# Kernel tuning notes

Hardware: AMD Instinct MI355X
Metric: run time of the kernel (lower is better)

## Reference

```python
import jax, jax.numpy as jnp
import numpy as np

B, S, H = 1, 4096, 2048
NH, HD = 16, 128  # num_heads, head_dim = H // NH


def setup_inputs() -> dict:
    key = jax.random.key(0)
    k1, k2, k3 = jax.random.split(key, 3)
    x = jax.random.normal(k1, (B, S, H), dtype=jnp.float32)
    w_qkv = jax.random.normal(k2, (3 * H, H), dtype=jnp.float32) * (1.0 / np.sqrt(H))
    w_out = jax.random.normal(k3, (H, H), dtype=jnp.float32) * (1.0 / np.sqrt(H))
    return {"x": x, "w_qkv": w_qkv, "w_out": w_out}


def reference(x, w_qkv, w_out):
    b, s, _ = x.shape
    # qkv projection: torch Linear computes x @ W^T
    qkv = jnp.einsum('bsh,oh->bso', x, w_qkv)
    qkv = qkv.reshape(b, s, 3, NH, HD).transpose(2, 0, 3, 1, 4)  # [3,B,NH,S,HD]
    q, k, v = qkv[0], qkv[1], qkv[2]
    # world_size == 1 -> single ring step == full attention with online softmax
    scores = jnp.einsum('bhqd,bhkd->bhqk', q, k) / np.sqrt(HD)
    m = jnp.max(scores, axis=-1, keepdims=True)          # running max (single step)
    p = jnp.exp(scores - m)                              # scores_exp
    out = jnp.einsum('bhqk,bhkd->bhqd', p, v)
    denom = jnp.sum(p, axis=-1, keepdims=True) + 1e-8    # running_sum + eps
    out = out / denom
    out = out.transpose(0, 2, 1, 3).reshape(b, s, H)     # [B,S,H]
    return jnp.einsum('bsh,oh->bso', out, w_out)
```

## Files before the change

### kernel.cpp

```cpp
#include <hip/hip_runtime.h>
#include <stdint.h>

typedef __attribute__((ext_vector_type(4))) float f32x4;
typedef __attribute__((ext_vector_type(16))) float f32x16;
typedef __attribute__((ext_vector_type(8))) short bf16x8;
typedef unsigned short u16;

#define MFMA(a, b, c) __builtin_amdgcn_mfma_f32_16x16x32_bf16(a, b, c, 0, 0, 0)
#define MFMA32(a, b, c) __builtin_amdgcn_mfma_f32_32x32x16_bf16(a, b, c, 0, 0, 0)
#define EXP2(x) __builtin_amdgcn_exp2f(x)
#define FENCE asm volatile("" ::: "memory")
#define BARRIER do { FENCE; __builtin_amdgcn_s_barrier(); FENCE; } while (0)

__device__ __forceinline__ u16 f2bf(float f) {
  union { float f; unsigned u; } x; x.f = f;
  unsigned r = x.u + 0x7fffu + ((x.u >> 16) & 1u);
  return (u16)(r >> 16);
}

__device__ __forceinline__ unsigned cvtpk(float lo, float hi) {
  unsigned r;
  asm("v_cvt_pk_bf16_f32 %0, %1, %2" : "=v"(r) : "v"(lo), "v"(hi));
  return r;
}

__device__ __forceinline__ void pl32swap(unsigned& a, unsigned& b) {
  asm volatile("v_permlane32_swap_b32 %0, %1" : "+v"(a), "+v"(b));
}

__device__ __forceinline__ void gload16(const void* g, void* l) {
  __builtin_amdgcn_global_load_lds(
      (const __attribute__((address_space(1))) unsigned int*)g,
      (__attribute__((address_space(3))) unsigned int*)l, 16, 0, 0);
}

__global__ void __launch_bounds__(256) cast_bf16(const float* __restrict__ in,
                                                 u16* __restrict__ out, int n4) {
  int i = blockIdx.x * 256 + threadIdx.x;
  if (i >= n4) return;
  float4 v = reinterpret_cast<const float4*>(in)[i];
  ushort4 o;
  o.x = f2bf(v.x); o.y = f2bf(v.y); o.z = f2bf(v.z); o.w = f2bf(v.w);
  reinterpret_cast<ushort4*>(out)[i] = o;
}

template <int EPI>
__global__ void __launch_bounds__(512)
gemm8(const u16* __restrict__ A, const u16* __restrict__ B,
      void* __restrict__ C0, void* __restrict__ C1, void* __restrict__ C2,
      int M, int N, int K, int MBt) {
  __shared__ alignas(16) char smb[98304];
  const int tid = threadIdx.x;
  const int w = tid >> 6, lane = tid & 63;
  const int lr = lane & 15, g = lane >> 4;
  const int wm = w >> 2, wn = w & 3;
  const int gb = (blockIdx.x & 7) * ((int)gridDim.x >> 3) + (blockIdx.x >> 3);
  const int mb = gb % MBt, nb = gb / MBt;
  const int m0 = mb * 128, n0 = nb * 256;
  const int NT = K >> 6, NIT = NT >> 1;

  const int l8 = lane >> 3, l7 = lane & 7;
  const int csb = (l7 ^ l8) * 16;
  const char* asrc;
  unsigned adst;
  {
    int r = (w & 3) * 8 + ((w >> 2) << 6) + l8;
    asrc = (const char*)(A + (size_t)(m0 + r) * K) + csb;
    adst = (unsigned)(r * 128 + l7 * 16);
  }
  const char* bsrcb[2];
  unsigned bdst[2];
#pragma unroll
  for (int j = 0; j < 2; ++j) {
    int c = 2 * w + j;
    int r = (c & 3) * 8 + ((c >> 2) << 6) + l8;
    bsrcb[j] = (const char*)(B + (size_t)(n0 + r) * K) + csb;
    bdst[j] = (unsigned)(r * 128 + l7 * 16);
  }
  const size_t row32 = (size_t)32 * K * 2;

#define STG(kt, u)                                                               \
  do {                                                                           \
    if ((kt) < NT) {                                                             \
      size_t _ko = (size_t)(kt) * 128;                                           \
      int _da = ((kt) & 1) ? 16384 : 0;                                          \
      int _db = 32768 + (((kt) & 1) ? 32768 : 0);                                \
      if ((u) == 0) {                                                            \
        gload16(asrc + _ko, smb + _da + adst);                                   \
      } else if ((u) == 1) {                                                     \
        gload16(bsrcb[0] + _ko, smb + _db + bdst[0]);                            \
        gload16(bsrcb[1] + _ko, smb + _db + bdst[1]);                            \
      } else if ((u) == 2) {                                                     \
        gload16(asrc + row32 + _ko, smb + _da + 4096 + adst);                    \
      } else {                                                                   \
        gload16(bsrcb[0] + row32 + _ko, smb + _db + 4096 + bdst[0]);             \
        gload16(bsrcb[1] + row32 + _ko, smb + _db + 4096 + bdst[1]);             \
      }                                                                          \
    }                                                                            \
  } while (0)

  f32x4 acc[4][4];
#pragma unroll
  for (int x = 0; x < 4; ++x)
#pragma unroll
    for (int y = 0; y < 4; ++y) acc[x][y] = f32x4{0.f, 0.f, 0.f, 0.f};
  bf16x8 af[2][2], bf01[2][2], bf23[2][2];
  const int aoff0 = ((g) ^ (lr & 7)) << 4;
  const int aoff1 = ((4 + g) ^ (lr & 7)) << 4;
  const int arowb = (wm * 64 + lr) * 128;
  const int browb = (wn * 64 + lr) * 128;

  auto LDA = [&](const char* base, int mih) {
#pragma unroll
    for (int mi = 0; mi < 2; ++mi) {
      const char* p = base + arowb + (mih * 32 + mi * 16) * 128;
      af[mi][0] = *(const bf16x8*)(p + aoff0);
      af[mi][1] = *(const bf16x8*)(p + aoff1);
    }
  };
  auto LDB = [&](const char* base, bf16x8 (*bfr)[2], int nih) {
#pragma unroll
    for (int ni = 0; ni < 2; ++ni) {
      const char* p = base + browb + (nih * 32 + ni * 16) * 128;
      bfr[ni][0] = *(const bf16x8*)(p + aoff0);
      bfr[ni][1] = *(const bf16x8*)(p + aoff1);
    }
  };
  auto MM = [&](int mih, int nih, bf16x8 (*bfr)[2]) {
    __builtin_amdgcn_s_setprio(1);
#pragma unroll
    for (int mi = 0; mi < 2; ++mi)
#pragma unroll
      for (int ni = 0; ni < 2; ++ni) {
        acc[mih * 2 + mi][nih * 2 + ni] =
            MFMA(af[mi][0], bfr[ni][0], acc[mih * 2 + mi][nih * 2 + ni]);
        acc[mih * 2 + mi][nih * 2 + ni] =
            MFMA(af[mi][1], bfr[ni][1], acc[mih * 2 + mi][nih * 2 + ni]);
      }
    __builtin_amdgcn_s_setprio(0);
  };

  STG(0, 0); STG(0, 1); STG(0, 2); STG(0, 3);
  STG(1, 0); STG(1, 1); STG(1, 2);
  asm volatile("s_waitcnt vmcnt(4)" ::: "memory");
  BARRIER;

  const char* A0 = smb;
  const char* A1 = smb + 16384;
  const char* B0 = smb + 32768;
  const char* B1 = smb + 65536;

  for (int it = 0; it < NIT; ++it) {
    const int t0 = 2 * it;
    const bool lastit = (it == NIT - 1);
    LDA(A0, 0); LDB(B0, bf01, 0); STG(t0 + 1, 3);
    BARRIER; MM(0, 0, bf01); BARRIER;
    LDB(B0, bf23, 1); STG(t0 + 2, 0);
    BARRIER; MM(0, 1, bf23); BARRIER;
    LDA(A0, 1); STG(t0 + 2, 1);
    BARRIER; MM(1, 1, bf23); BARRIER;
    STG(t0 + 2, 2);
    if (lastit) asm volatile("s_waitcnt vmcnt(0)" ::: "memory");
    else        asm volatile("s_waitcnt vmcnt(4)" ::: "memory");
    BARRIER; MM(1, 0, bf01); BARRIER;
    LDA(A1, 0); LDB(B1, bf01, 0); STG(t0 + 2, 3);
    BARRIER; MM(0, 0, bf01); BARRIER;
    LDB(B1, bf23, 1); STG(t0 + 3, 0);
    BARRIER; MM(0, 1, bf23); BARRIER;
    LDA(A1, 1); STG(t0 + 3, 1);
    BARRIER; MM(1, 1, bf23); BARRIER;
    STG(t0 + 3, 2);
    asm volatile("s_waitcnt vmcnt(4)" ::: "memory");
    BARRIER; MM(1, 0, bf01); BARRIER;
  }
#undef STG

  if (EPI == 0) {
    const float qs = 0.08838834764831845f * 1.4426950408889634f;
    u16* qo = (u16*)C0;
    u16* ko = (u16*)C1;
    u16* vo = (u16*)C2;
#pragma unroll
    for (int a = 0; a < 4; ++a) {
      int s0 = m0 + wm * 64 + a * 16 + g * 4;
#pragma unroll
      for (int b = 0; b < 4; ++b) {
        int n = n0 + wn * 64 + b * 16 + lr;
        int t = n >> 11, hh = (n >> 7) & 15, d = n & 127;
        if (t == 2) {
          ushort4 pk;
          pk.x = f2bf(acc[a][b][0]);
          pk.y = f2bf(acc[a][b][1]);
          pk.z = f2bf(acc[a][b][2]);
          pk.w = f2bf(acc[a][b][3]);
          *(ushort4*)(vo + (size_t)(hh * 128 + d) * 4096 + s0) = pk;
        } else {
          float sc = (t == 0) ? qs : 1.f;
          u16* dq = (t == 0 ? qo : ko) + (size_t)(hh * 4096 + s0) * 128 + d;
#pragma unroll
          for (int j = 0; j < 4; ++j) dq[(size_t)j * 128] = f2bf(acc[a][b][j] * sc);
        }
      }
    }
  } else {
    float* C = (float*)C0;
#pragma unroll
    for (int a = 0; a < 4; ++a)
#pragma unroll
      for (int b = 0; b < 4; ++b) {
        size_t r0 = (size_t)(m0 + wm * 64 + a * 16 + g * 4);
        int cn = n0 + wn * 64 + b * 16 + lr;
#pragma unroll
        for (int j = 0; j < 4; ++j) C[(r0 + j) * N + cn] = acc[a][b][j];
      }
  }
}

__global__ void __launch_bounds__(512)
attn_kernel(const u16* __restrict__ qg, const u16* __restrict__ kg,
            const u16* __restrict__ vtg, u16* __restrict__ og) {
  __shared__ alignas(64) char smb[131072];
  const int tid = threadIdx.x;
  const int w = tid >> 6, lane = tid & 63;
  const int ql = lane & 31, hl = lane >> 5;
  const int gb = (blockIdx.x & 7) * 32 + (blockIdx.x >> 3);
  const int h = gb >> 4;
  const int qb = gb & 15;

  const u16* ssrc[8];
  unsigned sdst[8];
  size_t sstep;
  if (w < 4) {
    sstep = 128 * 128;
#pragma unroll
    for (int i = 0; i < 8; ++i) {
      int c = w * 8 + i;
      int r = c * 4 + (lane >> 4);
      int sb = (lane & 15) ^ (r & 15);
      ssrc[i] = kg + (size_t)(h * 4096 + r) * 128 + sb * 8;
      sdst[i] = c * 1024;
    }
  } else {
    sstep = 128;
#pragma unroll
    for (int i = 0; i < 8; ++i) {
      int c = (w - 4) * 8 + i;
      int r = c * 4 + (lane >> 4);
      int sb = (lane & 15) ^ (r & 15);
      ssrc[i] = vtg + (size_t)(h * 128 + r) * 4096 + sb * 8;
      sdst[i] = 65536 + c * 1024;
    }
  }

  const u16* qrow = qg + (size_t)(h * 4096 + qb * 256 + w * 32 + ql) * 128 + hl * 8;
  bf16x8 qf[8];
#pragma unroll
  for (int s = 0; s < 8; ++s) qf[s] = *(const bf16x8*)(qrow + s * 16);

  f32x16 of[4];
#pragma unroll
  for (int i = 0; i < 4; ++i)
#pragma unroll
    for (int r = 0; r < 16; ++r) of[i][r] = 0.f;
  float mrun = -1e30f, lsum = 0.f;
  const float thr = 6.0f;

#pragma unroll
  for (int i = 0; i < 8; ++i) gload16(ssrc[i], smb + sdst[i]);

  const int kxor = (ql & 15) << 4;
  for (int t = 0; t < 32; ++t) {
    const int cur = t & 1;
    asm volatile("s_waitcnt vmcnt(0)" ::: "memory");
    __builtin_amdgcn_s_barrier();
    FENCE;
    if (t + 1 < 32) {
      const int nb = (t + 1) & 1;
#pragma unroll
      for (int i = 0; i < 8; ++i)
        gload16(ssrc[i] + (size_t)(t + 1) * sstep, smb + sdst[i] + nb * 32768);
    }
    const char* kbuf = smb + cur * 32768;
    const char* vbuf = smb + 65536 + cur * 32768;

    f32x16 st[4];
#pragma unroll
    for (int kb = 0; kb < 4; ++kb)
#pragma unroll
      for (int r = 0; r < 16; ++r) st[kb][r] = 0.f;
    __builtin_amdgcn_s_setprio(1);
#pragma unroll
    for (int s = 0; s < 8; ++s) {
      int off = ((s * 2 + hl) << 4) ^ kxor;
      bf16x8 k0 = *(const bf16x8*)(kbuf + (0 * 32 + ql) * 256 + off);
      bf16x8 k1 = *(const bf16x8*)(kbuf + (1 * 32 + ql) * 256 + off);
      bf16x8 k2 = *(const bf16x8*)(kbuf + (2 * 32 + ql) * 256 + off);
      bf16x8 k3 = *(const bf16x8*)(kbuf + (3 * 32 + ql) * 256 + off);
      st[0] = MFMA32(k0, qf[s], st[0]);
      st[1] = MFMA32(k1, qf[s], st[1]);
      st[2] = MFMA32(k2, qf[s], st[2]);
      st[3] = MFMA32(k3, qf[s], st[3]);
    }
    __builtin_amdgcn_s_setprio(0);

    float tmax = -1e30f;
#pragma unroll
    for (int kb = 0; kb < 4; ++kb)
#pragma unroll
      for (int r = 0; r < 16; ++r) tmax = fmaxf(tmax, st[kb][r]);
    tmax = fmaxf(tmax, __shfl_xor(tmax, 32));
    if (!__all(tmax - mrun <= thr)) {
      float mnew = fmaxf(mrun, tmax);
      float esc = EXP2(mrun - mnew);
#pragma unroll
      for (int db = 0; db < 4; ++db)
#pragma unroll
        for (int r = 0; r < 16; ++r) of[db][r] *= esc;
      lsum *= esc;
      mrun = mnew;
    }
    float psum = 0.f;
    union U { unsigned u[4]; bf16x8 v; };
    U paf[8];
#pragma unroll
    for (int gp = 0; gp < 2; ++gp) {
      unsigned pk0[8], pk1[8];
#pragma unroll
      for (int i = 0; i < 8; ++i) {
        float a0 = EXP2(st[2 * gp + 0][2 * i] - mrun);
        float b0 = EXP2(st[2 * gp + 0][2 * i + 1] - mrun);
        float a1 = EXP2(st[2 * gp + 1][2 * i] - mrun);
        float b1 = EXP2(st[2 * gp + 1][2 * i + 1] - mrun);
        psum += (a0 + b0) + (a1 + b1);
        pk0[i] = cvtpk(a0, b0);
        pk1[i] = cvtpk(a1, b1);
      }
      pl32swap(pk0[0], pk0[2]); pl32swap(pk0[1], pk0[3]);
      pl32swap(pk0[4], pk0[6]); pl32swap(pk0[5], pk0[7]);
      pl32swap(pk1[0], pk1[2]); pl32swap(pk1[1], pk1[3]);
      pl32swap(pk1[4], pk1[6]); pl32swap(pk1[5], pk1[7]);
#pragma unroll
      for (int i = 0; i < 4; ++i) {
        paf[gp * 4 + 0].u[i] = pk0[i];
        paf[gp * 4 + 1].u[i] = pk0[4 + i];
        paf[gp * 4 + 2].u[i] = pk1[i];
        paf[gp * 4 + 3].u[i] = pk1[4 + i];
      }
    }
    psum += __shfl_xor(psum, 32);
    lsum += psum;

    __builtin_amdgcn_s_setprio(1);
#pragma unroll
    for (int db = 0; db < 4; ++db) {
      const char* vrow = vbuf + (db * 32 + ql) * 256;
#pragma unroll
      for (int kp = 0; kp < 8; ++kp) {
        int m = (kp * 2 + hl) ^ (ql & 15);
        bf16x8 vf = *(const bf16x8*)(vrow + m * 16);
        of[db] = MFMA32(vf, paf[kp].v, of[db]);
      }
    }
    __builtin_amdgcn_s_setprio(0);
    FENCE;
  }

  float linv = 1.f / (lsum + 1e-8f);
  size_t qrow_o = (size_t)(qb * 256 + w * 32 + ql) * 2048 + h * 128;
#pragma unroll
  for (int db = 0; db < 4; ++db)
#pragma unroll
    for (int u = 0; u < 4; ++u) {
      ushort4 pk;
      pk.x = f2bf(of[db][4 * u + 0] * linv);
      pk.y = f2bf(of[db][4 * u + 1] * linv);
      pk.z = f2bf(of[db][4 * u + 2] * linv);
      pk.w = f2bf(of[db][4 * u + 3] * linv);
      *(ushort4*)(og + qrow_o + db * 32 + 8 * u + hl * 4) = pk;
    }
}

extern "C" void kernel_launch(void* const* d_in, const int* in_sizes, int n_in,
                              void* d_out, int out_size, void* d_ws, size_t ws_size,
                              hipStream_t stream) {
  const float* x = (const float*)d_in[0];
  const float* w_qkv = (const float*)d_in[1];
  const float* w_out = (const float*)d_in[2];

  char* ws = (char*)d_ws;
  u16* xb = (u16*)(ws + 0);
  u16* wqkvb = (u16*)(ws + 16777216);
  u16* woutb = (u16*)(ws + 41943040);
  u16* qb = (u16*)(ws + 50331648);
  u16* kb = (u16*)(ws + 67108864);
  u16* vtb = (u16*)(ws + 83886080);
  u16* aob = (u16*)(ws + 100663296);

  cast_bf16<<<8192, 256, 0, stream>>>(x, xb, 2097152);
  cast_bf16<<<12288, 256, 0, stream>>>(w_qkv, wqkvb, 3145728);
  cast_bf16<<<4096, 256, 0, stream>>>(w_out, woutb, 1048576);

  gemm8<0><<<768, 512, 0, stream>>>(xb, wqkvb, qb, kb, vtb, 4096, 6144, 2048, 32);
  attn_kernel<<<256, 512, 0, stream>>>(qb, kb, vtb, aob);
  gemm8<1><<<256, 512, 0, stream>>>(aob, woutb, d_out, nullptr, nullptr, 4096, 2048, 2048, 32);
}
```

Measured before the change: 314.5 us.

## Fuse bf16 casts into one kernel and restructure GEMM k-loop pipeline

Replaces the three separate fp32-to-bf16 cast launches with one grid-stride kernel covering all three tensors, which removes two kernel launches. The GEMM main loop is rescheduled so each phase loads both B halves, issues several global-to-LDS stages together, and runs two MFMA groups per barrier pair. This halves the number of barriers per k-tile and changes the vmcnt waits. The reordered stage issue and wait counts carry a risk of subtle hazards on LDS buffers.

```diff
diff --git a/kernel.cpp b/kernel.cpp
--- a/kernel.cpp
+++ b/kernel.cpp
@@ -34,14 +34,22 @@
       (__attribute__((address_space(3))) unsigned int*)l, 16, 0, 0);
 }
 
-__global__ void __launch_bounds__(256) cast_bf16(const float* __restrict__ in,
-                                                 u16* __restrict__ out, int n4) {
-  int i = blockIdx.x * 256 + threadIdx.x;
-  if (i >= n4) return;
-  float4 v = reinterpret_cast<const float4*>(in)[i];
-  ushort4 o;
-  o.x = f2bf(v.x); o.y = f2bf(v.y); o.z = f2bf(v.z); o.w = f2bf(v.w);
-  reinterpret_cast<ushort4*>(out)[i] = o;
+__global__ void __launch_bounds__(256)
+cast_all(const float* __restrict__ x, const float* __restrict__ wq,
+         const float* __restrict__ wo, u16* __restrict__ xb,
+         u16* __restrict__ wqb, u16* __restrict__ wob) {
+  for (int idx = blockIdx.x * 256 + threadIdx.x; idx < 6291456; idx += 256 * 2048) {
+    const float* in;
+    u16* out;
+    int j;
+    if (idx < 2097152) { in = x; out = xb; j = idx; }
+    else if (idx < 5242880) { in = wq; out = wqb; j = idx - 2097152; }
+    else { in = wo; out = wob; j = idx - 5242880; }
+    float4 v = reinterpret_cast<const float4*>(in)[j];
+    ushort4 o;
+    o.x = f2bf(v.x); o.y = f2bf(v.y); o.z = f2bf(v.z); o.w = f2bf(v.w);
+    reinterpret_cast<ushort4*>(out)[j] = o;
+  }
 }
 
 template <int EPI>
@@ -98,6 +106,7 @@
       }                                                                          \
     }                                                                            \
   } while (0)
+#define VMC(n) asm volatile("s_waitcnt vmcnt(" #n ")" ::: "memory")
 
   f32x4 acc[4][4];
 #pragma unroll
@@ -127,7 +136,6 @@
     }
   };
   auto MM = [&](int mih, int nih, bf16x8 (*bfr)[2]) {
-    __builtin_amdgcn_s_setprio(1);
 #pragma unroll
     for (int mi = 0; mi < 2; ++mi)
 #pragma unroll
@@ -137,12 +145,11 @@
         acc[mih * 2 + mi][nih * 2 + ni] =
             MFMA(af[mi][1], bfr[ni][1], acc[mih * 2 + mi][nih * 2 + ni]);
       }
-    __builtin_amdgcn_s_setprio(0);
   };
 
   STG(0, 0); STG(0, 1); STG(0, 2); STG(0, 3);
-  STG(1, 0); STG(1, 1); STG(1, 2);
-  asm volatile("s_waitcnt vmcnt(4)" ::: "memory");
+  STG(1, 0); STG(1, 1); STG(1, 3);
+  VMC(5);
   BARRIER;
 
   const char* A0 = smb;
@@ -152,28 +159,34 @@
 
   for (int it = 0; it < NIT; ++it) {
     const int t0 = 2 * it;
-    const bool lastit = (it == NIT - 1);
-    LDA(A0, 0); LDB(B0, bf01, 0); STG(t0 + 1, 3);
-    BARRIER; MM(0, 0, bf01); BARRIER;
-    LDB(B0, bf23, 1); STG(t0 + 2, 0);
-    BARRIER; MM(0, 1, bf23); BARRIER;
-    LDA(A0, 1); STG(t0 + 2, 1);
-    BARRIER; MM(1, 1, bf23); BARRIER;
+    const bool last = (it == NIT - 1);
+    LDA(A0, 0); LDB(B0, bf01, 0); LDB(B0, bf23, 1);
+    STG(t0 + 1, 2);
+    VMC(6);
+    BARRIER;
+    __builtin_amdgcn_s_setprio(1); MM(0, 0, bf01); MM(0, 1, bf23); __builtin_amdgcn_s_setprio(0);
+    BARRIER;
+    LDA(A0, 1);
+    STG(t0 + 2, 0); STG(t0 + 2, 1); STG(t0 + 2, 3);
+    if (last) VMC(1); else VMC(6);
+    BARRIER;
+    __builtin_amdgcn_s_setprio(1); MM(1, 1, bf23); MM(1, 0, bf01); __builtin_amdgcn_s_setprio(0);
+    BARRIER;
+    LDA(A1, 0); LDB(B1, bf01, 0); LDB(B1, bf23, 1);
     STG(t0 + 2, 2);
-    if (lastit) asm volatile("s_waitcnt vmcnt(0)" ::: "memory");
-    else        asm volatile("s_waitcnt vmcnt(4)" ::: "memory");
-    BARRIER; MM(1, 0, bf01); BARRIER;
-    LDA(A1, 0); LDB(B1, bf01, 0); STG(t0 + 2, 3);
-    BARRIER; MM(0, 0, bf01); BARRIER;
-    LDB(B1, bf23, 1); STG(t0 + 3, 0);
-    BARRIER; MM(0, 1, bf23); BARRIER;
-    LDA(A1, 1); STG(t0 + 3, 1);
-    BARRIER; MM(1, 1, bf23); BARRIER;
-    STG(t0 + 3, 2);
-    asm volatile("s_waitcnt vmcnt(4)" ::: "memory");
-    BARRIER; MM(1, 0, bf01); BARRIER;
+    if (last) VMC(0); else VMC(6);
+    BARRIER;
+    __builtin_amdgcn_s_setprio(1); MM(0, 0, bf01); MM(0, 1, bf23); __builtin_amdgcn_s_setprio(0);
+    BARRIER;
+    LDA(A1, 1);
+    STG(t0 + 3, 0); STG(t0 + 3, 1); STG(t0 + 3, 3);
+    if (last) VMC(0); else VMC(6);
+    BARRIER;
+    __builtin_amdgcn_s_setprio(1); MM(1, 1, bf23); MM(1, 0, bf01); __builtin_amdgcn_s_setprio(0);
+    BARRIER;
   }
 #undef STG
+#undef VMC
 
   if (EPI == 0) {
     const float qs = 0.08838834764831845f * 1.4426950408889634f;
@@ -396,10 +409,7 @@
   u16* vtb = (u16*)(ws + 83886080);
   u16* aob = (u16*)(ws + 100663296);
 
-  cast_bf16<<<8192, 256, 0, stream>>>(x, xb, 2097152);
-  cast_bf16<<<12288, 256, 0, stream>>>(w_qkv, wqkvb, 3145728);
-  cast_bf16<<<4096, 256, 0, stream>>>(w_out, woutb, 1048576);
-
+  cast_all<<<2048, 256, 0, stream>>>(x, w_qkv, w_out, xb, wqkvb, woutb);
   gemm8<0><<<768, 512, 0, stream>>>(xb, wqkvb, qb, kb, vtb, 4096, 6144, 2048, 32);
   attn_kernel<<<256, 512, 0, stream>>>(qb, kb, vtb, aob);
   gemm8<1><<<256, 512, 0, stream>>>(aob, woutb, d_out, nullptr, nullptr, 4096, 2048, 2048, 32);
```

Result: no change. 312.3 us (-0.7%).
